# Kernel optimization log

Measured on AMD Instinct MI355X. Metric: run time of the kernel, lower is better.

The kernel has to match this reference:

```python
import jax, jax.numpy as jnp
import numpy as np

N, E, F_IN, D, EF, L, G = 50000, 800000, 92, 64, 50, 3, 128
EPS = 1e-5


def setup_inputs() -> dict:
    key = jax.random.key(0)
    ks = jax.random.split(key, 16)
    Z = 2 * D + EF  # concat dim for CGConv messages
    inp = {
        "x": jax.random.normal(ks[0], (N, F_IN), dtype=jnp.float32),
        "edge_index": jax.random.randint(ks[1], (2, E), 0, N, dtype=jnp.int32),
        "edge_attr": jax.random.uniform(ks[2], (E, EF), dtype=jnp.float32),
        "batch": jnp.sort(jax.random.randint(ks[3], (N,), 0, G, dtype=jnp.int32)),
        "pre_W": jax.random.normal(ks[4], (F_IN, D), dtype=jnp.float32) * 0.05,
        "pre_b": jnp.zeros((D,), jnp.float32),
        "Wf": jax.random.normal(ks[5], (L, Z, D), dtype=jnp.float32) * 0.05,
        "bf": jnp.zeros((L, D), jnp.float32),
        "Ws": jax.random.normal(ks[6], (L, Z, D), dtype=jnp.float32) * 0.05,
        "bs": jnp.zeros((L, D), jnp.float32),
        "bn_gamma": jnp.ones((L, D), jnp.float32) + 0.1 * jax.random.normal(ks[7], (L, D), dtype=jnp.float32),
        "bn_beta": 0.1 * jax.random.normal(ks[8], (L, D), dtype=jnp.float32),
        "bn_mean": 0.1 * jax.random.normal(ks[9], (L, D), dtype=jnp.float32),
        "bn_var": jax.random.uniform(ks[10], (L, D), dtype=jnp.float32, minval=0.5, maxval=1.5),
        "post_W": jax.random.normal(ks[11], (D, D), dtype=jnp.float32) * 0.05,
        "post_b": jnp.zeros((D,), jnp.float32),
        "out_W": jax.random.normal(ks[12], (D, 1), dtype=jnp.float32) * 0.05,
        "out_b": jnp.zeros((1,), jnp.float32),
    }
    return inp


def reference(x, edge_index, edge_attr, batch, pre_W, pre_b, Wf, bf, Ws, bs,
              bn_gamma, bn_beta, bn_mean, bn_var, post_W, post_b, out_W, out_b):
    src = edge_index[0]  # x_j (source)
    dst = edge_index[1]  # x_i (target, aggregation index)

    # pre FC + relu
    h = jax.nn.relu(x @ pre_W + pre_b)

    # in-degree for mean aggregation
    deg = jax.ops.segment_sum(jnp.ones((E,), h.dtype), dst, num_segments=N)
    deg = jnp.maximum(deg, 1.0)[:, None]

    for l in range(L):
        # CGConv: z_ij = [h_i || h_j || e_ij]
        z = jnp.concatenate([h[dst], h[src], edge_attr], axis=-1)  # [E, 2D+EF]
        m = jax.nn.sigmoid(z @ Wf[l] + bf[l]) * jax.nn.softplus(z @ Ws[l] + bs[l])
        agg = jax.ops.segment_sum(m, dst, num_segments=N) / deg
        h = h + agg  # residual in CGConv
        # BatchNorm1d (eval mode, running stats); dropout is identity in eval
        h = bn_gamma[l] * (h - bn_mean[l]) * jax.lax.rsqrt(bn_var[l] + EPS) + bn_beta[l]

    # early global_mean_pool over graphs
    cnt = jax.ops.segment_sum(jnp.ones((N,), h.dtype), batch, num_segments=G)
    cnt = jnp.maximum(cnt, 1.0)[:, None]
    g = jax.ops.segment_sum(h, batch, num_segments=G) / cnt  # [G, D]

    g = jax.nn.relu(g @ post_W + post_b)
    return g @ out_W + out_b  # [G, 1]
```

## Files before the change

### kernel.cpp

```cpp
#include <hip/hip_runtime.h>
#include <cmath>

#define N_NODES 50000
#define N_EDGES 800000
#define F_IN 92
#define DIM 64
#define EF 50
#define NLAYER 3
#define NGRAPH 128
#define ZROWS 178

__global__ __launch_bounds__(256, 3) void pre_fc(const float* __restrict__ x,
                                                 const float* __restrict__ W,
                                                 const float* __restrict__ b,
                                                 float* __restrict__ h, int N)
{
    const int lane = threadIdx.x & 63;
    const int wid  = blockIdx.x * (blockDim.x >> 6) + (threadIdx.x >> 6);
    const int nw   = gridDim.x * (blockDim.x >> 6);
    float w[F_IN];
#pragma unroll
    for (int k = 0; k < F_IN; ++k) w[k] = W[k * DIM + lane];
    const float bb = b[lane];
#pragma unroll 1
    for (int n = wid; n < N; n += nw) {
        const int nu = __builtin_amdgcn_readfirstlane(n);
        const float* xr = x + (size_t)nu * F_IN;
        float a = bb;
#pragma unroll
        for (int k = 0; k < F_IN; ++k) a = fmaf(xr[k], w[k], a);
        h[(size_t)nu * DIM + lane] = fmaxf(a, 0.f);
    }
}

__global__ __launch_bounds__(256) void deg_cnt(const int* __restrict__ ei, int E,
                                               const int* __restrict__ batch, int N,
                                               float* __restrict__ deg,
                                               float* __restrict__ cnt)
{
    const int i = blockIdx.x * blockDim.x + threadIdx.x;
    const int stride = gridDim.x * blockDim.x;
    for (int e = i; e < E; e += stride) unsafeAtomicAdd(&deg[ei[E + e]], 1.f);
    for (int n = i; n < N; n += stride) unsafeAtomicAdd(&cnt[batch[n]], 1.f);
}

__global__ __launch_bounds__(256, 2) void node_proj(const float* __restrict__ h,
                                                    const float* __restrict__ Wfl,
                                                    const float* __restrict__ Wsl,
                                                    const float* __restrict__ bf,
                                                    const float* __restrict__ bs,
                                                    float* __restrict__ Pd,
                                                    float* __restrict__ Ps, int N)
{
    const int lane = threadIdx.x & 63;
    const int wid  = blockIdx.x * (blockDim.x >> 6) + (threadIdx.x >> 6);
    const int nw   = gridDim.x * (blockDim.x >> 6);
    const int half = wid & 1;
    const float* wfb = Wfl + (half ? DIM * DIM : 0);
    const float* wsb = Wsl + (half ? DIM * DIM : 0);
    float wf[DIM], ws[DIM];
#pragma unroll
    for (int k = 0; k < DIM; ++k) { wf[k] = wfb[k * DIM + lane]; ws[k] = wsb[k * DIM + lane]; }
    const float b0 = half ? 0.f : bf[lane];
    const float b1 = half ? 0.f : bs[lane];
    float* P = half ? Ps : Pd;
#pragma unroll 1
    for (int n = (wid >> 1); n < N; n += (nw >> 1)) {
        const int nu = __builtin_amdgcn_readfirstlane(n);
        const float* hr = h + (size_t)nu * DIM;
        float a0 = b0, a1 = b1;
#pragma unroll
        for (int k = 0; k < DIM; ++k) {
            const float v = hr[k];
            a0 = fmaf(v, wf[k], a0);
            a1 = fmaf(v, ws[k], a1);
        }
        P[(size_t)nu * 128 + lane]      = a0;
        P[(size_t)nu * 128 + 64 + lane] = a1;
    }
}

#define EA_PAD 51
#define TP_PAD 129
__global__ __launch_bounds__(512) void edge_fused(const int* __restrict__ ei,
                                                  const float* __restrict__ eattr,
                                                  const float* __restrict__ Pd,
                                                  const float* __restrict__ Ps,
                                                  const float* __restrict__ WfE,
                                                  const float* __restrict__ WsE,
                                                  float* __restrict__ agg, int E)
{
    __shared__ float ea_lds[64 * EA_PAD];
    __shared__ float out_lds[64 * TP_PAD];

    const int tid = threadIdx.x;
    const int e0  = blockIdx.x * 64;

    {
        const float* src = eattr + (size_t)e0 * EF;
        for (int idx = tid; idx < 64 * EF; idx += 512) {
            const int e = idx / EF;
            const int k = idx - e * EF;
            ea_lds[e * EA_PAD + k] = src[idx];
        }
    }
    __syncthreads();

    {
        const int e  = tid & 63;
        const int wv = __builtin_amdgcn_readfirstlane(tid >> 6);
        const float* Wbase = (wv < 4) ? WfE : WsE;
        const int c0 = (wv & 3) * 16;
        const int cb = ((wv < 4) ? 0 : 64) + c0;

        float acc[16];
#pragma unroll
        for (int j = 0; j < 16; ++j) acc[j] = 0.f;

        const float* ear = ea_lds + e * EA_PAD;
#pragma unroll 5
        for (int k = 0; k < EF; ++k) {
            const float eak = ear[k];
            const float* wr = Wbase + k * DIM + c0;
#pragma unroll
            for (int j = 0; j < 16; ++j) acc[j] = fmaf(eak, wr[j], acc[j]);
        }
        float* orow = out_lds + e * TP_PAD + cb;
#pragma unroll
        for (int j = 0; j < 16; ++j) orow[j] = acc[j];
    }
    __syncthreads();

    {
        const int lane = tid & 63;
        const int wv   = __builtin_amdgcn_readfirstlane(tid >> 6);
#pragma unroll 2
        for (int i = 0; i < 8; ++i) {
            const int el = wv * 8 + i;
            const int eg = e0 + el;
            const int s  = ei[eg];
            const int d  = ei[E + eg];
            const float pf  = out_lds[el * TP_PAD + lane];
            const float psv = out_lds[el * TP_PAD + 64 + lane];
            const float* pdr = Pd + (size_t)d * 128;
            const float* psr = Ps + (size_t)s * 128;
            const float zf = pf  + pdr[lane]      + psr[lane];
            const float zs = psv + pdr[64 + lane] + psr[64 + lane];
            const float sig = 1.f / (1.f + __expf(-zf));
            const float sp  = fmaxf(zs, 0.f) + __logf(1.f + __expf(-fabsf(zs)));
            unsafeAtomicAdd(&agg[(size_t)d * DIM + lane], sig * sp);
        }
    }
}

__global__ __launch_bounds__(256) void node_update(float* __restrict__ h,
                                                   const float* __restrict__ agg,
                                                   const float* __restrict__ deg,
                                                   const float* __restrict__ gamma,
                                                   const float* __restrict__ beta,
                                                   const float* __restrict__ mean,
                                                   const float* __restrict__ var, int N)
{
    const int lane = threadIdx.x & 63;
    const float g  = gamma[lane];
    const float bt = beta[lane];
    const float mn = mean[lane];
    const float iv = rsqrtf(var[lane] + 1e-5f);
    const int idx = blockIdx.x * blockDim.x + threadIdx.x;
    const int stride = gridDim.x * blockDim.x;
    const int total = N * DIM;
    for (int i = idx; i < total; i += stride) {
        const int n = i >> 6;
        const float inv = 1.f / fmaxf(deg[n], 1.f);
        const float v = h[i] + agg[i] * inv;
        h[i] = fmaf(g, (v - mn) * iv, bt);
    }
}

__global__ __launch_bounds__(256) void pool_sum(const float* __restrict__ h,
                                                const int* __restrict__ batch,
                                                float* __restrict__ gsum, int N)
{
    const int lane = threadIdx.x & 63;
    const int wid  = blockIdx.x * (blockDim.x >> 6) + (threadIdx.x >> 6);
    const int nw   = gridDim.x * (blockDim.x >> 6);
    for (int n = wid; n < N; n += nw) {
        const int nu = __builtin_amdgcn_readfirstlane(n);
        const int b = batch[nu];
        unsafeAtomicAdd(&gsum[(size_t)b * DIM + lane], h[(size_t)nu * DIM + lane]);
    }
}

__global__ __launch_bounds__(64) void head(const float* __restrict__ gsum,
                                           const float* __restrict__ cnt,
                                           const float* __restrict__ postW,
                                           const float* __restrict__ postb,
                                           const float* __restrict__ outW,
                                           const float* __restrict__ outb,
                                           float* __restrict__ out)
{
    const int gi = blockIdx.x;
    const int lane = threadIdx.x;
    const float inv = 1.f / fmaxf(cnt[gi], 1.f);
    const float gval = gsum[(size_t)gi * DIM + lane] * inv;
    float acc = postb[lane];
#pragma unroll
    for (int k = 0; k < DIM; ++k) acc = fmaf(__shfl(gval, k, 64), postW[k * DIM + lane], acc);
    const float t = fmaxf(acc, 0.f);
    float prod = t * outW[lane];
#pragma unroll
    for (int off = 32; off > 0; off >>= 1) prod += __shfl_down(prod, off, 64);
    if (lane == 0) out[gi] = prod + outb[0];
}

extern "C" void kernel_launch(void* const* d_in, const int* in_sizes, int n_in,
                              void* d_out, int out_size, void* d_ws, size_t ws_size,
                              hipStream_t stream)
{
    const float* x     = (const float*)d_in[0];
    const int*   ei    = (const int*)d_in[1];
    const float* eattr = (const float*)d_in[2];
    const int*   batch = (const int*)d_in[3];
    const float* preW  = (const float*)d_in[4];
    const float* preb  = (const float*)d_in[5];
    const float* Wf    = (const float*)d_in[6];
    const float* bf    = (const float*)d_in[7];
    const float* Ws    = (const float*)d_in[8];
    const float* bs    = (const float*)d_in[9];
    const float* gamma = (const float*)d_in[10];
    const float* beta  = (const float*)d_in[11];
    const float* mean  = (const float*)d_in[12];
    const float* var   = (const float*)d_in[13];
    const float* postW = (const float*)d_in[14];
    const float* postb = (const float*)d_in[15];
    const float* outW  = (const float*)d_in[16];
    const float* outb  = (const float*)d_in[17];
    float* out = (float*)d_out;

    const int N = N_NODES, E = N_EDGES, G = NGRAPH;

    char* p = (char*)d_ws;
    float* h    = (float*)p; p += (size_t)N * DIM * 4;
    float* Pd   = (float*)p; p += (size_t)N * 128 * 4;
    float* Ps   = (float*)p; p += (size_t)N * 128 * 4;
    float* agg  = (float*)p; p += (size_t)N * DIM * 4;
    float* deg  = (float*)p; p += (size_t)N * 4;
    float* gsum = (float*)p; p += (size_t)G * DIM * 4;
    float* cnt  = (float*)p; p += (size_t)G * 4;

    hipMemsetAsync(deg, 0, ((size_t)N + G * DIM + G) * 4, stream);

    pre_fc<<<512, 256, 0, stream>>>(x, preW, preb, h, N);
    deg_cnt<<<512, 256, 0, stream>>>(ei, E, batch, N, deg, cnt);

    for (int l = 0; l < NLAYER; ++l) {
        const float* Wfl = Wf + (size_t)l * ZROWS * DIM;
        const float* Wsl = Ws + (size_t)l * ZROWS * DIM;
        hipMemsetAsync(agg, 0, (size_t)N * DIM * 4, stream);
        node_proj<<<512, 256, 0, stream>>>(h, Wfl, Wsl, bf + l * DIM, bs + l * DIM, Pd, Ps, N);
        edge_fused<<<E / 64, 512, 0, stream>>>(ei, eattr, Pd, Ps,
                                               Wfl + 2 * DIM * DIM, Wsl + 2 * DIM * DIM, agg, E);
        node_update<<<1024, 256, 0, stream>>>(h, agg, deg, gamma + l * DIM, beta + l * DIM,
                                              mean + l * DIM, var + l * DIM, N);
    }

    pool_sum<<<512, 256, 0, stream>>>(h, batch, gsum, N);
    head<<<G, 64, 0, stream>>>(gsum, cnt, postW, postb, outW, outb, out);
}
```

Measured before the change: 1.056 ms.

## Sort edges by destination (CSR) and pre-reduce messages before atomics

Adds a counting sort of edges by destination: an integer histogram, a single-block prefix scan and a scatter pass that produce sorted src/dst/edge-id arrays. The edge kernel reads these sorted arrays and accumulates consecutive messages for the same destination in registers, issuing one atomic per run instead of one per edge. The aim is fewer global float atomics and better locality for the destination-row loads. In exchange, edge attributes are now gathered through the edge-id permutation instead of read contiguously, and the preprocessing adds a serial single-block scan plus an atomic-based scatter on every call.

```diff
diff --git a/kernel.cpp b/kernel.cpp
--- a/kernel.cpp
+++ b/kernel.cpp
@@ -33,15 +33,56 @@
     }
 }
 
-__global__ __launch_bounds__(256) void deg_cnt(const int* __restrict__ ei, int E,
-                                               const int* __restrict__ batch, int N,
-                                               float* __restrict__ deg,
-                                               float* __restrict__ cnt)
+__global__ __launch_bounds__(256) void hist_cnt(const int* __restrict__ ei, int E,
+                                                const int* __restrict__ batch, int N,
+                                                int* __restrict__ hist,
+                                                float* __restrict__ cnt)
 {
     const int i = blockIdx.x * blockDim.x + threadIdx.x;
     const int stride = gridDim.x * blockDim.x;
-    for (int e = i; e < E; e += stride) unsafeAtomicAdd(&deg[ei[E + e]], 1.f);
+    for (int e = i; e < E; e += stride) atomicAdd(&hist[ei[E + e]], 1);
     for (int n = i; n < N; n += stride) unsafeAtomicAdd(&cnt[batch[n]], 1.f);
+}
+
+__global__ __launch_bounds__(256) void scan_offs(const int* __restrict__ hist,
+                                                 int* __restrict__ offs, int Nn)
+{
+    __shared__ int ssum[256];
+    const int t = threadIdx.x;
+    const int seg = (Nn + 255) / 256;
+    const int lo = t * seg;
+    const int hi = (lo + seg < Nn) ? lo + seg : Nn;
+    int s = 0;
+    for (int i = lo; i < hi; ++i) s += hist[i];
+    ssum[t] = s;
+    __syncthreads();
+    if (t == 0) {
+        int run = 0;
+        for (int i = 0; i < 256; ++i) { int v = ssum[i]; ssum[i] = run; run += v; }
+        offs[Nn] = run;
+    }
+    __syncthreads();
+    int run = ssum[t];
+    for (int i = lo; i < hi; ++i) { offs[i] = run; run += hist[i]; }
+}
+
+__global__ __launch_bounds__(256) void scatter_edges(const int* __restrict__ ei,
+                                                     const int* __restrict__ offs,
+                                                     int* __restrict__ cursor,
+                                                     int* __restrict__ s_src,
+                                                     int* __restrict__ s_dst,
+                                                     int* __restrict__ s_eid, int E)
+{
+    const int i = blockIdx.x * blockDim.x + threadIdx.x;
+    const int stride = gridDim.x * blockDim.x;
+    for (int e = i; e < E; e += stride) {
+        const int d = ei[E + e];
+        const int s = ei[e];
+        const int pos = offs[d] + atomicAdd(&cursor[d], 1);
+        s_src[pos] = s;
+        s_dst[pos] = d;
+        s_eid[pos] = e;
+    }
 }
 
 __global__ __launch_bounds__(256, 2) void node_proj(const float* __restrict__ h,
@@ -82,7 +123,9 @@
 
 #define EA_PAD 51
 #define TP_PAD 129
-__global__ __launch_bounds__(512) void edge_fused(const int* __restrict__ ei,
+__global__ __launch_bounds__(512) void edge_fused(const int* __restrict__ s_src,
+                                                  const int* __restrict__ s_dst,
+                                                  const int* __restrict__ s_eid,
                                                   const float* __restrict__ eattr,
                                                   const float* __restrict__ Pd,
                                                   const float* __restrict__ Ps,
@@ -97,11 +140,11 @@
     const int e0  = blockIdx.x * 64;
 
     {
-        const float* src = eattr + (size_t)e0 * EF;
+        const int* eid = s_eid + e0;
         for (int idx = tid; idx < 64 * EF; idx += 512) {
             const int e = idx / EF;
             const int k = idx - e * EF;
-            ea_lds[e * EA_PAD + k] = src[idx];
+            ea_lds[e * EA_PAD + k] = eattr[(size_t)eid[e] * EF + k];
         }
     }
     __syncthreads();
@@ -134,28 +177,39 @@
     {
         const int lane = tid & 63;
         const int wv   = __builtin_amdgcn_readfirstlane(tid >> 6);
-#pragma unroll 2
+        const int base = e0 + wv * 8;
+
+        int dcur = s_dst[base];
+        const float* pdr = Pd + (size_t)dcur * 128;
+        float pd0 = pdr[lane], pd1 = pdr[64 + lane];
+        float acc = 0.f;
+#pragma unroll
         for (int i = 0; i < 8; ++i) {
             const int el = wv * 8 + i;
-            const int eg = e0 + el;
-            const int s  = ei[eg];
-            const int d  = ei[E + eg];
-            const float pf  = out_lds[el * TP_PAD + lane];
-            const float psv = out_lds[el * TP_PAD + 64 + lane];
-            const float* pdr = Pd + (size_t)d * 128;
-            const float* psr = Ps + (size_t)s * 128;
-            const float zf = pf  + pdr[lane]      + psr[lane];
-            const float zs = psv + pdr[64 + lane] + psr[64 + lane];
+            const int eg = base + i;
+            const int dd = s_dst[eg];
+            const int ss = s_src[eg];
+            if (dd != dcur) {
+                unsafeAtomicAdd(&agg[(size_t)dcur * DIM + lane], acc);
+                acc = 0.f;
+                dcur = dd;
+                pdr = Pd + (size_t)dcur * 128;
+                pd0 = pdr[lane]; pd1 = pdr[64 + lane];
+            }
+            const float* psr = Ps + (size_t)ss * 128;
+            const float zf = out_lds[el * TP_PAD + lane]      + pd0 + psr[lane];
+            const float zs = out_lds[el * TP_PAD + 64 + lane] + pd1 + psr[64 + lane];
             const float sig = 1.f / (1.f + __expf(-zf));
             const float sp  = fmaxf(zs, 0.f) + __logf(1.f + __expf(-fabsf(zs)));
-            unsafeAtomicAdd(&agg[(size_t)d * DIM + lane], sig * sp);
+            acc = fmaf(sig, sp, acc);
         }
+        unsafeAtomicAdd(&agg[(size_t)dcur * DIM + lane], acc);
     }
 }
 
 __global__ __launch_bounds__(256) void node_update(float* __restrict__ h,
                                                    const float* __restrict__ agg,
-                                                   const float* __restrict__ deg,
+                                                   const int* __restrict__ hist,
                                                    const float* __restrict__ gamma,
                                                    const float* __restrict__ beta,
                                                    const float* __restrict__ mean,
@@ -171,7 +225,7 @@
     const int total = N * DIM;
     for (int i = idx; i < total; i += stride) {
         const int n = i >> 6;
-        const float inv = 1.f / fmaxf(deg[n], 1.f);
+        const float inv = 1.f / fmaxf((float)hist[n], 1.f);
         const float v = h[i] + agg[i] * inv;
         h[i] = fmaf(g, (v - mn) * iv, bt);
     }
@@ -240,27 +294,35 @@
     const int N = N_NODES, E = N_EDGES, G = NGRAPH;
 
     char* p = (char*)d_ws;
-    float* h    = (float*)p; p += (size_t)N * DIM * 4;
-    float* Pd   = (float*)p; p += (size_t)N * 128 * 4;
-    float* Ps   = (float*)p; p += (size_t)N * 128 * 4;
-    float* agg  = (float*)p; p += (size_t)N * DIM * 4;
-    float* deg  = (float*)p; p += (size_t)N * 4;
-    float* gsum = (float*)p; p += (size_t)G * DIM * 4;
-    float* cnt  = (float*)p; p += (size_t)G * 4;
-
-    hipMemsetAsync(deg, 0, ((size_t)N + G * DIM + G) * 4, stream);
+    float* h      = (float*)p; p += (size_t)N * DIM * 4;
+    float* Pd     = (float*)p; p += (size_t)N * 128 * 4;
+    float* Ps     = (float*)p; p += (size_t)N * 128 * 4;
+    float* agg    = (float*)p; p += (size_t)N * DIM * 4;
+    float* gsum   = (float*)p; p += (size_t)G * DIM * 4;
+    float* cnt    = (float*)p; p += (size_t)G * 4;
+    int*   hist   = (int*)p;   p += (size_t)N * 4;
+    int*   cursor = (int*)p;   p += (size_t)N * 4;
+    int*   offs   = (int*)p;   p += (size_t)(N + 1) * 4;
+    int*   s_src  = (int*)p;   p += (size_t)E * 4;
+    int*   s_dst  = (int*)p;   p += (size_t)E * 4;
+    int*   s_eid  = (int*)p;   p += (size_t)E * 4;
+
+    hipMemsetAsync(gsum, 0, ((size_t)G * DIM + G + N + N) * 4, stream);
+
+    hist_cnt<<<512, 256, 0, stream>>>(ei, E, batch, N, hist, cnt);
+    scan_offs<<<1, 256, 0, stream>>>(hist, offs, N);
+    scatter_edges<<<512, 256, 0, stream>>>(ei, offs, cursor, s_src, s_dst, s_eid, E);
 
     pre_fc<<<512, 256, 0, stream>>>(x, preW, preb, h, N);
-    deg_cnt<<<512, 256, 0, stream>>>(ei, E, batch, N, deg, cnt);
 
     for (int l = 0; l < NLAYER; ++l) {
         const float* Wfl = Wf + (size_t)l * ZROWS * DIM;
         const float* Wsl = Ws + (size_t)l * ZROWS * DIM;
         hipMemsetAsync(agg, 0, (size_t)N * DIM * 4, stream);
         node_proj<<<512, 256, 0, stream>>>(h, Wfl, Wsl, bf + l * DIM, bs + l * DIM, Pd, Ps, N);
-        edge_fused<<<E / 64, 512, 0, stream>>>(ei, eattr, Pd, Ps,
+        edge_fused<<<E / 64, 512, 0, stream>>>(s_src, s_dst, s_eid, eattr, Pd, Ps,
                                                Wfl + 2 * DIM * DIM, Wsl + 2 * DIM * DIM, agg, E);
-        node_update<<<1024, 256, 0, stream>>>(h, agg, deg, gamma + l * DIM, beta + l * DIM,
+        node_update<<<1024, 256, 0, stream>>>(h, agg, hist, gamma + l * DIM, beta + l * DIM,
                                               mean + l * DIM, var + l * DIM, N);
     }
 
```

New measurement: 1.187 ms (median of 2 runs). 1.12x slower.
